# Performance work log

Hardware: AMD Instinct MI355X
Metric: run time of the kernel (lower is better)

## Reference

```python
import jax, jax.numpy as jnp
import numpy as np
from jax import lax

K = 5
SCALE = 100.0
IN_CHN = 128
OUT_CHN = 128
KS = 3
STRIDE = 1
PAD = 1
N_W = OUT_CHN * IN_CHN * KS * KS


def setup_inputs() -> dict:
    key = jax.random.key(0)
    k1, k2, k3, k4, k5 = jax.random.split(key, 5)
    x = jax.random.normal(k1, (32, IN_CHN, 56, 56), dtype=jnp.float32)
    Alpha = jax.random.uniform(k2, (OUT_CHN, 1, 1), dtype=jnp.float32)
    # xavier-normal-ish init for M, Z
    M = jax.random.normal(k3, (OUT_CHN, IN_CHN, KS, KS), dtype=jnp.float32) * 0.05
    Z = jax.random.normal(k4, (K, OUT_CHN, IN_CHN, KS, KS), dtype=jnp.float32) * 0.05
    # rv ~ N(0, 1/sqrt(scale)) of shape (1, K); sample is all-zeros so the random branch is taken
    rv = jax.random.normal(k5, (1, K), dtype=jnp.float32) / np.float32(np.sqrt(SCALE))
    return {"x": x, "Alpha": Alpha, "M": M, "Z": Z, "rv": rv}


def reference(x, Alpha, M, Z, rv):
    # --- SDP weight synthesis (normalization is done under no_grad in torch) ---
    m = M.reshape(N_W)                # (N,)
    z = Z.reshape(K, N_W)             # (K, N)
    A = m * m + jnp.sum(z * z, axis=0) / SCALE
    inv = lax.rsqrt(A)
    m_n = m * inv
    z_n = z * inv
    w = (rv @ z_n + m_n).reshape(OUT_CHN, IN_CHN, KS, KS)  # (O,I,k,k)
    # --- sign binarization of weights and activations (ReCU) ---
    bw = jnp.sign(w)
    ba = jnp.sign(x)
    # --- conv2d, NCHW/OIHW ---
    out = lax.conv_general_dilated(
        ba, bw,
        window_strides=(STRIDE, STRIDE),
        padding=[(PAD, PAD), (PAD, PAD)],
        dimension_numbers=("NCHW", "OIHW", "NCHW"),
    )
    out = out * Alpha  # Alpha (O,1,1) broadcasts over (B,O,H,W)
    return out
```

## Files before the change

kernel.cpp:

```cpp
#include <hip/hip_runtime.h>
#include <stdint.h>

typedef unsigned int u32;
typedef unsigned long long u64;

#define HW      3136
#define PADW    58
#define PADHW   3364

#define WB_OFF   0
#define BF_OFF   18432
#define N2A_OFF  23040
#define AB_OFF   23552

__global__ __launch_bounds__(256) void k_prep(
    const float* __restrict__ x, const float* __restrict__ Alpha,
    const float* __restrict__ M, const float* __restrict__ Z,
    const float* __restrict__ rv, char* __restrict__ ws)
{
  int t = threadIdx.x;
  if (blockIdx.x < 128) {
    u32*   wb  = (u32*)(ws + WB_OFF);
    float* Bf  = (float*)(ws + BF_OFF);
    float* n2a = (float*)(ws + N2A_OFF);
    __shared__ float sw[1152];
    __shared__ u32 sbits[36];
    __shared__ int spc[9];
    int o = blockIdx.x;
    float r0 = rv[0], r1 = rv[1], r2 = rv[2], r3 = rv[3], r4 = rv[4];
    const float4* M4 = (const float4*)M;
    const float4* Z4 = (const float4*)Z;
    float4* sw4 = (float4*)sw;

    for (int j = t; j < 288; j += 256) {
      float4 a = M4[o * 288 + j];
      float4 z;
      z = Z4[0 * 36864 + o * 288 + j];
      a.x = fmaf(r0, z.x, a.x); a.y = fmaf(r0, z.y, a.y);
      a.z = fmaf(r0, z.z, a.z); a.w = fmaf(r0, z.w, a.w);
      z = Z4[1 * 36864 + o * 288 + j];
      a.x = fmaf(r1, z.x, a.x); a.y = fmaf(r1, z.y, a.y);
      a.z = fmaf(r1, z.z, a.z); a.w = fmaf(r1, z.w, a.w);
      z = Z4[2 * 36864 + o * 288 + j];
      a.x = fmaf(r2, z.x, a.x); a.y = fmaf(r2, z.y, a.y);
      a.z = fmaf(r2, z.z, a.z); a.w = fmaf(r2, z.w, a.w);
      z = Z4[3 * 36864 + o * 288 + j];
      a.x = fmaf(r3, z.x, a.x); a.y = fmaf(r3, z.y, a.y);
      a.z = fmaf(r3, z.z, a.z); a.w = fmaf(r3, z.w, a.w);
      z = Z4[4 * 36864 + o * 288 + j];
      a.x = fmaf(r4, z.x, a.x); a.y = fmaf(r4, z.y, a.y);
      a.z = fmaf(r4, z.z, a.z); a.w = fmaf(r4, z.w, a.w);
      sw4[j] = a;
    }
    __syncthreads();

    if (t < 36) {
      int tap = t >> 2;
      int wd  = t & 3;
      u32 bits = 0;
#pragma unroll
      for (int c = 0; c < 32; ++c) {
        float v = sw[(wd * 32 + c) * 9 + tap];
        bits |= (v > 0.0f ? 1u : 0u) << c;
      }
      wb[(o * 9 + tap) * 4 + wd] = bits;
      sbits[t] = bits;
    }
    __syncthreads();
    if (t < 9)
      spc[t] = __popc(sbits[4 * t]) + __popc(sbits[4 * t + 1])
             + __popc(sbits[4 * t + 2]) + __popc(sbits[4 * t + 3]);
    __syncthreads();
    if (t < 9) {
      int ht = t / 3, wt = t - ht * 3;
      int corr = 0;
#pragma unroll
      for (int tap = 0; tap < 9; ++tap) {
        int dh = tap / 3, dw = tap - dh * 3;
        int inv = ((ht == 0) & (dh == 0)) | ((ht == 2) & (dh == 2)) |
                  ((wt == 0) & (dw == 0)) | ((wt == 2) & (dw == 2));
        if (inv) corr += 128 - 2 * spc[tap];
      }
      Bf[t * 128 + o] = (float)(1152 - corr) * Alpha[o];
    }
    if (t == 0) n2a[o] = -2.0f * Alpha[o];
  } else {
    u32* abw  = (u32*)(ws + AB_OFF);
    int bidx  = blockIdx.x - 128;
    int chunk = bidx % 53;
    int b     = bidx / 53;
    int px    = chunk * 64 + (t & 63);
    int g     = t >> 6;
    if (px >= PADHW) return;
    int ph = px / PADW;
    int pw = px - ph * PADW;
    u32 bits = 0;
    if (ph >= 1 && ph <= 56 && pw >= 1 && pw <= 56) {
      const float* xp = x + (size_t)b * (128 * HW) + (size_t)g * (32 * HW)
                          + (ph - 1) * 56 + (pw - 1);
#pragma unroll
      for (int c = 0; c < 32; ++c)
        bits |= (xp[(size_t)c * HW] > 0.0f ? 1u : 0u) << c;
    }
    abw[((size_t)b * PADHW + px) * 4 + g] = bits;
  }
}

__global__ __launch_bounds__(256) void k_conv(
    const char* __restrict__ ws, float* __restrict__ out)
{
  const uint4*  ab  = (const uint4*)(ws + AB_OFF);
  const uint4*  wbg = (const uint4*)(ws + WB_OFF);
  const float*  BfG = (const float*)(ws + BF_OFF);
  const float*  n2a = (const float*)(ws + N2A_OFF);

  __shared__ float sBf[9][8];
  int tid = threadIdx.x;
  int bx  = blockIdx.x;
  int og  = bx / 98;
  int o0  = og * 8;
  if (tid < 72) {
    int cl = tid / 8, oi = tid - cl * 8;
    sBf[cl][oi] = BfG[cl * 128 + o0 + oi];
  }
  __syncthreads();

  int q  = (bx - og * 98) * 256 + tid;
  int b  = q / 784;
  int r  = q - b * 784;
  int h  = r / 14;
  int w4 = r - h * 14;
  int w0 = w4 * 4;

  const uint4* ap = ab + ((size_t)b * PADW + h) * PADW + w0;
  u32 A[3][6][4];
#pragma unroll
  for (int rr = 0; rr < 3; ++rr)
#pragma unroll
    for (int cc = 0; cc < 6; ++cc) {
      uint4 v = ap[(size_t)rr * PADW + cc];
      A[rr][cc][0] = v.x; A[rr][cc][1] = v.y;
      A[rr][cc][2] = v.z; A[rr][cc][3] = v.w;
    }

  int ht  = (h == 0) ? 0 : (h == 55 ? 6 : 3);
  int cl0 = ht + ((w0 == 0) ? 0 : 1);
  int cl1 = ht + 1;
  int cl3 = ht + ((w0 == 52) ? 2 : 1);

  float* outp = out + ((size_t)b * 128 + o0) * HW + h * 56 + w0;

#pragma unroll
  for (int oi = 0; oi < 8; ++oi) {
    int o = o0 + oi;
    int s0 = 0, s1 = 0, s2 = 0, s3 = 0;
#pragma unroll
    for (int dh = 0; dh < 3; ++dh)
#pragma unroll
      for (int dw = 0; dw < 3; ++dw) {
        uint4 wv = wbg[o * 9 + dh * 3 + dw];
#pragma unroll
        for (int k = 0; k < 4; ++k) {
          u32 wk = (&wv.x)[k];
          s0 += __popc(A[dh][dw + 0][k] ^ wk);
          s1 += __popc(A[dh][dw + 1][k] ^ wk);
          s2 += __popc(A[dh][dw + 2][k] ^ wk);
          s3 += __popc(A[dh][dw + 3][k] ^ wk);
        }
      }
    float na = n2a[o];
    float4 ov;
    ov.x = fmaf((float)s0, na, sBf[0][oi] + (sBf[cl0][oi] - sBf[0][oi]));
    ov.x = fmaf((float)s0, na, sBf[cl0][oi]);
    ov.y = fmaf((float)s1, na, sBf[cl1][oi]);
    ov.z = fmaf((float)s2, na, sBf[cl1][oi]);
    ov.w = fmaf((float)s3, na, sBf[cl3][oi]);
    *(float4*)(outp + (size_t)oi * HW) = ov;
  }
}

extern "C" void kernel_launch(void* const* d_in, const int* in_sizes, int n_in,
                              void* d_out, int out_size, void* d_ws, size_t ws_size,
                              hipStream_t stream)
{
  const float* x     = (const float*)d_in[0];
  const float* Alpha = (const float*)d_in[1];
  const float* M     = (const float*)d_in[2];
  const float* Z     = (const float*)d_in[3];
  const float* rv    = (const float*)d_in[4];
  float* out         = (float*)d_out;
  char*  ws          = (char*)d_ws;

  k_prep<<<128 + 32 * 53, 256, 0, stream>>>(x, Alpha, M, Z, rv, ws);
  k_conv<<<16 * 98, 256, 0, stream>>>(ws, out);
}
```

Measured before the change: 136.5 us.

## Replace XOR-popcount binary conv with int8 MFMA implicit GEMM

```diff
diff --git a/kernel.cpp b/kernel.cpp
--- a/kernel.cpp
+++ b/kernel.cpp
@@ -2,30 +2,28 @@
 #include <stdint.h>
 
 typedef unsigned int u32;
-typedef unsigned long long u64;
+typedef int v4i  __attribute__((ext_vector_type(4)));
+typedef int v16i __attribute__((ext_vector_type(16)));
 
 #define HW      3136
 #define PADW    58
 #define PADHW   3364
 
-#define WB_OFF   0
-#define BF_OFF   18432
-#define N2A_OFF  23040
-#define AB_OFF   23552
+#define WA_OFF   0
+#define AI8_OFF  147456
+
+#define NB_W     128
+#define NB_A     1792
+#define NB_R     228
 
 __global__ __launch_bounds__(256) void k_prep(
-    const float* __restrict__ x, const float* __restrict__ Alpha,
-    const float* __restrict__ M, const float* __restrict__ Z,
-    const float* __restrict__ rv, char* __restrict__ ws)
+    const float* __restrict__ x, const float* __restrict__ M,
+    const float* __restrict__ Z, const float* __restrict__ rv,
+    char* __restrict__ ws)
 {
   int t = threadIdx.x;
-  if (blockIdx.x < 128) {
-    u32*   wb  = (u32*)(ws + WB_OFF);
-    float* Bf  = (float*)(ws + BF_OFF);
-    float* n2a = (float*)(ws + N2A_OFF);
+  if (blockIdx.x < NB_W) {
     __shared__ float sw[1152];
-    __shared__ u32 sbits[36];
-    __shared__ int spc[9];
     int o = blockIdx.x;
     float r0 = rv[0], r1 = rv[1], r2 = rv[2], r3 = rv[3], r4 = rv[4];
     const float4* M4 = (const float4*)M;
@@ -54,128 +52,122 @@
     }
     __syncthreads();
 
-    if (t < 36) {
-      int tap = t >> 2;
-      int wd  = t & 3;
-      u32 bits = 0;
+    if (t < 72) {
+      int tap   = t >> 3;
+      int kq    = (t & 7) >> 1;
+      int khalf = t & 1;
+      union { char c[16]; uint4 v; } u;
 #pragma unroll
-      for (int c = 0; c < 32; ++c) {
-        float v = sw[(wd * 32 + c) * 9 + tap];
-        bits |= (v > 0.0f ? 1u : 0u) << c;
+      for (int j = 0; j < 16; ++j) {
+        int c = kq * 32 + khalf * 16 + j;
+        u.c[j] = (sw[c * 9 + tap] > 0.0f) ? (char)1 : (char)-1;
       }
-      wb[(o * 9 + tap) * 4 + wd] = bits;
-      sbits[t] = bits;
+      int og   = o >> 5;
+      int lane = (o & 31) + 32 * khalf;
+      uint4* wa = (uint4*)(ws + WA_OFF);
+      wa[((og * 9 + tap) * 4 + kq) * 64 + lane] = u.v;
+    }
+  } else if (blockIdx.x < NB_W + NB_A) {
+    __shared__ float sA[56 * 128];
+    int bidx = blockIdx.x - NB_W;
+    int b = bidx / 56;
+    int h = bidx - b * 56;
+    int c    = t >> 1;
+    int half = t & 1;
+    const float4* xp = (const float4*)(x + ((size_t)(b * 128 + c) * HW + h * 56 + half * 28));
+#pragma unroll
+    for (int j = 0; j < 7; ++j) {
+      float4 f = xp[j];
+      int w = half * 28 + j * 4;
+      sA[(w + 0) * 128 + c] = f.x;
+      sA[(w + 1) * 128 + c] = f.y;
+      sA[(w + 2) * 128 + c] = f.z;
+      sA[(w + 3) * 128 + c] = f.w;
     }
     __syncthreads();
-    if (t < 9)
-      spc[t] = __popc(sbits[4 * t]) + __popc(sbits[4 * t + 1])
-             + __popc(sbits[4 * t + 2]) + __popc(sbits[4 * t + 3]);
-    __syncthreads();
-    if (t < 9) {
-      int ht = t / 3, wt = t - ht * 3;
-      int corr = 0;
+    uint4* dst = (uint4*)(ws + AI8_OFF + (((size_t)b * PADW + (h + 1)) * PADW + 1) * 128);
+    for (int i = t; i < 448; i += 256) {
+      int w  = i >> 3;
+      int cc = i & 7;
+      union { char c[16]; uint4 v; } u;
 #pragma unroll
-      for (int tap = 0; tap < 9; ++tap) {
-        int dh = tap / 3, dw = tap - dh * 3;
-        int inv = ((ht == 0) & (dh == 0)) | ((ht == 2) & (dh == 2)) |
-                  ((wt == 0) & (dw == 0)) | ((wt == 2) & (dw == 2));
-        if (inv) corr += 128 - 2 * spc[tap];
-      }
-      Bf[t * 128 + o] = (float)(1152 - corr) * Alpha[o];
+      for (int j = 0; j < 16; ++j)
+        u.c[j] = (sA[w * 128 + cc * 16 + j] > 0.0f) ? (char)1 : (char)-1;
+      dst[i] = u.v;
     }
-    if (t == 0) n2a[o] = -2.0f * Alpha[o];
   } else {
-    u32* abw  = (u32*)(ws + AB_OFF);
-    int bidx  = blockIdx.x - 128;
-    int chunk = bidx % 53;
-    int b     = bidx / 53;
-    int px    = chunk * 64 + (t & 63);
-    int g     = t >> 6;
-    if (px >= PADHW) return;
-    int ph = px / PADW;
-    int pw = px - ph * PADW;
-    u32 bits = 0;
-    if (ph >= 1 && ph <= 56 && pw >= 1 && pw <= 56) {
-      const float* xp = x + (size_t)b * (128 * HW) + (size_t)g * (32 * HW)
-                          + (ph - 1) * 56 + (pw - 1);
-#pragma unroll
-      for (int c = 0; c < 32; ++c)
-        bits |= (xp[(size_t)c * HW] > 0.0f ? 1u : 0u) << c;
+    int e = (blockIdx.x - NB_W - NB_A) * 256 + t;
+    int wd  = e & 7;
+    int pxr = (e >> 3) % 228;
+    int b   = (e >> 3) / 228;
+    int pp;
+    if      (pxr < 58)  pp = pxr;
+    else if (pxr < 116) pp = 57 * PADW + (pxr - 58);
+    else {
+      int s = pxr - 116;
+      pp = (1 + (s >> 1)) * PADW + ((s & 1) ? 57 : 0);
     }
-    abw[((size_t)b * PADHW + px) * 4 + g] = bits;
+    uint4* dst = (uint4*)(ws + AI8_OFF);
+    dst[((size_t)b * PADHW + pp) * 8 + wd] = make_uint4(0, 0, 0, 0);
   }
 }
 
-__global__ __launch_bounds__(256) void k_conv(
-    const char* __restrict__ ws, float* __restrict__ out)
+__global__ __launch_bounds__(256, 1) void k_conv(
+    const char* __restrict__ ws, const float* __restrict__ Alpha,
+    float* __restrict__ out)
 {
-  const uint4*  ab  = (const uint4*)(ws + AB_OFF);
-  const uint4*  wbg = (const uint4*)(ws + WB_OFF);
-  const float*  BfG = (const float*)(ws + BF_OFF);
-  const float*  n2a = (const float*)(ws + N2A_OFF);
+  int tid   = threadIdx.x;
+  int lane  = tid & 63;
+  int wv    = tid >> 6;
+  int og    = blockIdx.y;
+  int khalf = lane >> 5;
+  int ln    = lane & 31;
 
-  __shared__ float sBf[9][8];
-  int tid = threadIdx.x;
-  int bx  = blockIdx.x;
-  int og  = bx / 98;
-  int o0  = og * 8;
-  if (tid < 72) {
-    int cl = tid / 8, oi = tid - cl * 8;
-    sBf[cl][oi] = BfG[cl * 128 + o0 + oi];
-  }
-  __syncthreads();
+  const v4i* wa = (const v4i*)(ws + WA_OFF) + (size_t)og * 36 * 64 + lane;
+  v4i A[36];
+#pragma unroll
+  for (int f = 0; f < 36; ++f) A[f] = wa[f * 64];
 
-  int q  = (bx - og * 98) * 256 + tid;
-  int b  = q / 784;
-  int r  = q - b * 784;
-  int h  = r / 14;
-  int w4 = r - h * 14;
-  int w0 = w4 * 4;
+  float alphaR[16];
+#pragma unroll
+  for (int r = 0; r < 16; ++r)
+    alphaR[r] = Alpha[og * 32 + (r & 3) + 8 * (r >> 2) + 4 * khalf];
 
-  const uint4* ap = ab + ((size_t)b * PADW + h) * PADW + w0;
-  u32 A[3][6][4];
+  const char* ai8 = ws + AI8_OFF;
+
 #pragma unroll
-  for (int rr = 0; rr < 3; ++rr)
+  for (int it = 0; it < 4; ++it) {
+    int tile = (blockIdx.x * 16 + wv * 4 + it);
+    int pxg  = tile * 32;
+    int b    = pxg / HW;
+    int pxb  = pxg - b * HW;
+    int px   = pxb + ln;
+    int h    = px / 56;
+    int w    = px - h * 56;
+    const char* ap = ai8 + (((size_t)b * PADW + (h + 1)) * PADW + (w + 1)) * 128
+                         + khalf * 16;
+
+    v16i acc = {0,0,0,0,0,0,0,0,0,0,0,0,0,0,0,0};
 #pragma unroll
-    for (int cc = 0; cc < 6; ++cc) {
-      uint4 v = ap[(size_t)rr * PADW + cc];
-      A[rr][cc][0] = v.x; A[rr][cc][1] = v.y;
-      A[rr][cc][2] = v.z; A[rr][cc][3] = v.w;
+    for (int dh = 0; dh < 3; ++dh) {
+#pragma unroll
+      for (int dw = 0; dw < 3; ++dw) {
+        const char* tp = ap + ((dh - 1) * PADW + (dw - 1)) * 128;
+        int tap = dh * 3 + dw;
+#pragma unroll
+        for (int kq = 0; kq < 4; ++kq) {
+          v4i Bf = *(const v4i*)(tp + kq * 32);
+          acc = __builtin_amdgcn_mfma_i32_32x32x32_i8(A[tap * 4 + kq], Bf, acc, 0, 0, 0);
+        }
+      }
     }
 
-  int ht  = (h == 0) ? 0 : (h == 55 ? 6 : 3);
-  int cl0 = ht + ((w0 == 0) ? 0 : 1);
-  int cl1 = ht + 1;
-  int cl3 = ht + ((w0 == 52) ? 2 : 1);
-
-  float* outp = out + ((size_t)b * 128 + o0) * HW + h * 56 + w0;
-
+    float* op = out + ((size_t)b * 128 + og * 32) * HW + pxb + ln;
 #pragma unroll
-  for (int oi = 0; oi < 8; ++oi) {
-    int o = o0 + oi;
-    int s0 = 0, s1 = 0, s2 = 0, s3 = 0;
-#pragma unroll
-    for (int dh = 0; dh < 3; ++dh)
-#pragma unroll
-      for (int dw = 0; dw < 3; ++dw) {
-        uint4 wv = wbg[o * 9 + dh * 3 + dw];
-#pragma unroll
-        for (int k = 0; k < 4; ++k) {
-          u32 wk = (&wv.x)[k];
-          s0 += __popc(A[dh][dw + 0][k] ^ wk);
-          s1 += __popc(A[dh][dw + 1][k] ^ wk);
-          s2 += __popc(A[dh][dw + 2][k] ^ wk);
-          s3 += __popc(A[dh][dw + 3][k] ^ wk);
-        }
-      }
-    float na = n2a[o];
-    float4 ov;
-    ov.x = fmaf((float)s0, na, sBf[0][oi] + (sBf[cl0][oi] - sBf[0][oi]));
-    ov.x = fmaf((float)s0, na, sBf[cl0][oi]);
-    ov.y = fmaf((float)s1, na, sBf[cl1][oi]);
-    ov.z = fmaf((float)s2, na, sBf[cl1][oi]);
-    ov.w = fmaf((float)s3, na, sBf[cl3][oi]);
-    *(float4*)(outp + (size_t)oi * HW) = ov;
+    for (int r = 0; r < 16; ++r) {
+      int olo = (r & 3) + 8 * (r >> 2) + 4 * khalf;
+      op[(size_t)olo * HW] = (float)acc[r] * alphaR[r];
+    }
   }
 }
 
@@ -191,6 +183,6 @@
   float* out         = (float*)d_out;
   char*  ws          = (char*)d_ws;
 
-  k_prep<<<128 + 32 * 53, 256, 0, stream>>>(x, Alpha, M, Z, rv, ws);
-  k_conv<<<16 * 98, 256, 0, stream>>>(ws, out);
+  k_prep<<<NB_W + NB_A + NB_R, 256, 0, stream>>>(x, M, Z, rv, ws);
+  k_conv<<<dim3(196, 4), 256, 0, stream>>>(ws, Alpha, out);
 }
```

New measurement: 181.3 us. 32.8% more time.
